# Optimization experiments

Hardware: AMD Instinct MI355X
Metric: run time of the kernel (lower is better)

Reference implementation:

```python
import jax, jax.numpy as jnp
import numpy as np

N = 50000      # nodes
E = 800000     # edges (avg degree 16)
IN = 128
H = 128
OUT = 1000
K = 10
EPS = 1e-5


def setup_inputs() -> dict:
    key = jax.random.key(0)
    ks = jax.random.split(key, 12)
    s = 0.05  # small init scale for weights
    return {
        "x": jax.random.normal(ks[0], (N, IN), jnp.float32),
        "edge_index": jax.random.randint(ks[1], (2, E), 0, N, dtype=jnp.int32),
        "W1": jax.random.normal(ks[2], (IN, H), jnp.float32) * s,
        "b1": jnp.zeros((H,), jnp.float32),
        "g1": jnp.ones((H,), jnp.float32),
        "be1": jnp.zeros((H,), jnp.float32),
        "W2": jax.random.normal(ks[3], (H, H), jnp.float32) * s,
        "b2": jnp.zeros((H,), jnp.float32),
        "g2": jnp.ones((H,), jnp.float32),
        "be2": jnp.zeros((H,), jnp.float32),
        "att": jax.random.uniform(ks[4], (K + 1,), jnp.float32),  # uniform_(0,1) init
        "W3": jax.random.normal(ks[5], (H, H // 2), jnp.float32) * s,
        "b3": jnp.zeros((H // 2,), jnp.float32),
        "g3": jnp.ones((H // 2,), jnp.float32),
        "be3": jnp.zeros((H // 2,), jnp.float32),
        "Wout": jax.random.normal(ks[6], (H // 2, OUT), jnp.float32) * s,
        "bout": jnp.zeros((OUT,), jnp.float32),
    }


def _bn(x, g, b):
    # training-mode BatchNorm1d: biased batch stats over the node dim
    m = jnp.mean(x, axis=0)
    v = jnp.var(x, axis=0)
    return g * (x - m) * jax.lax.rsqrt(v + EPS) + b


def reference(x, edge_index, W1, b1, g1, be1, W2, b2, g2, be2, att,
              W3, b3, g3, be3, Wout, bout):
    # input MLP with residual
    h = jax.nn.relu(_bn(x @ W1 + b1, g1, be1))
    identity = h
    h = jax.nn.relu(_bn(h @ W2 + b2, g2, be2)) + identity

    # DAGNN: K unnormalized scatter-add hops (APPNP.propagate with edge_weight=1),
    # then softmax(att)-weighted sum over hop representations. Accumulate the
    # weighted sum on the fly instead of materializing the [N, H, K+1] stack.
    src, dst = edge_index[0], edge_index[1]  # message flows src -> dst
    w = jax.nn.softmax(att)
    out = w[0] * h
    cur = h
    for i in range(K):
        cur = jax.ops.segment_sum(cur[src], dst, num_segments=N)
        out = out + w[i + 1] * cur

    # output MLP
    h3 = jax.nn.relu(_bn(out @ W3 + b3, g3, be3))
    return h3 @ Wout + bout
```

## Files before the change

### kernel.cpp

```cpp
#include <hip/hip_runtime.h>
#include <cstdint>
#include <cstddef>

#define N_NODES 50000
#define N_EDGES 800000
#define DIM_H   128
#define DIM_P   64
#define DIM_OUT 1000
#define OUT_PAD 1024
#define KHOPS   10
#define BN_EPS  1e-5f

static inline int ceil_div(int a, int b) { return (a + b - 1) / b; }

typedef short  bf16x8  __attribute__((ext_vector_type(8)));
typedef float  floatx4 __attribute__((ext_vector_type(4)));

__device__ __forceinline__ unsigned short f2bf_rne(float v) {
    unsigned int u = __float_as_uint(v);
    return (unsigned short)((u + 0x7fffu + ((u >> 16) & 1u)) >> 16);
}
__device__ __forceinline__ float bf2f(unsigned short u) {
    return __uint_as_float((unsigned int)u << 16);
}

__global__ void init_all(const float* __restrict__ att, float* __restrict__ w,
                         const float* __restrict__ Wout, unsigned short* __restrict__ WT,
                         double* __restrict__ st, int* __restrict__ deg) {
    const int gid = blockIdx.x * blockDim.x + threadIdx.x;
    const int stride = gridDim.x * blockDim.x;
    if (gid == 0) {
        float mx = att[0];
        for (int i = 1; i < KHOPS + 1; ++i) mx = fmaxf(mx, att[i]);
        float e[KHOPS + 1];
        float s = 0.f;
        for (int i = 0; i < KHOPS + 1; ++i) { e[i] = expf(att[i] - mx); s += e[i]; }
        for (int i = 0; i < KHOPS + 1; ++i) w[i] = e[i] / s;
    }
    for (int i = gid; i < 640; i += stride) st[i] = 0.0;
    for (int i = gid; i < N_NODES; i += stride) deg[i] = 0;
    for (int i = gid; i < OUT_PAD * DIM_P; i += stride) {
        int c = i >> 6, k = i & 63;
        WT[i] = (c < DIM_OUT) ? f2bf_rne(Wout[(size_t)k * DIM_OUT + c]) : (unsigned short)0;
    }
}

__global__ void count_deg(const int* __restrict__ dst, int* __restrict__ deg, int ne) {
    int i = blockIdx.x * blockDim.x + threadIdx.x;
    if (i < ne) atomicAdd(&deg[dst[i]], 1);
}

__global__ __launch_bounds__(1024) void scan_local(const int* __restrict__ deg,
                                                   int* __restrict__ row_ptr,
                                                   int* __restrict__ bsums, int n) {
    __shared__ int wsum[16];
    const int i = blockIdx.x * 1024 + threadIdx.x;
    const int lane = threadIdx.x & 63, w = threadIdx.x >> 6;
    int v = (i < n) ? deg[i] : 0;
    int s = v;
#pragma unroll
    for (int d = 1; d < 64; d <<= 1) {
        int t = __shfl_up(s, d, 64);
        if (lane >= d) s += t;
    }
    if (lane == 63) wsum[w] = s;
    __syncthreads();
    if (w == 0) {
        int x = (lane < 16) ? wsum[lane] : 0;
#pragma unroll
        for (int d = 1; d < 16; d <<= 1) {
            int t = __shfl_up(x, d, 64);
            if (lane >= d) x += t;
        }
        if (lane < 16) wsum[lane] = x;
    }
    __syncthreads();
    int incl = s + ((w > 0) ? wsum[w - 1] : 0);
    if (i < n) row_ptr[i + 1] = incl;
    if (threadIdx.x == 1023) bsums[blockIdx.x] = incl;
}

__global__ void scan_finish(int* __restrict__ row_ptr, int* __restrict__ deg,
                            const int* __restrict__ bsums, int n, int nb) {
    __shared__ int boff[64];
    if (threadIdx.x < 64) {
        int lane = threadIdx.x;
        int v = (lane < nb) ? bsums[lane] : 0;
        int s = v;
#pragma unroll
        for (int d = 1; d < 64; d <<= 1) {
            int t = __shfl_up(s, d, 64);
            if (lane >= d) s += t;
        }
        boff[lane] = s - v;
    }
    __syncthreads();
    int i = blockIdx.x * blockDim.x + threadIdx.x;
    if (i < n) {
        int incl = row_ptr[i + 1] + boff[i >> 10];
        row_ptr[i + 1] = incl;
        deg[i] = incl - deg[i];
    }
    if (i == 0) row_ptr[0] = 0;
}

__global__ void fill_csr(const int* __restrict__ src, const int* __restrict__ dst,
                         int* __restrict__ cursor, int* __restrict__ col, int ne) {
    int i = blockIdx.x * blockDim.x + threadIdx.x;
    if (i < ne) {
        int d = dst[i];
        int pos = atomicAdd(&cursor[d], 1);
        col[pos] = src[i];
    }
}

template<int KD, int CPB, bool OBF>
__global__ __launch_bounds__(256) void gemm_fused(
    const float* __restrict__ A,  const double* __restrict__ stA,
    const float* __restrict__ gA, const float* __restrict__ beA,
    const float* __restrict__ A2, const double* __restrict__ stA2,
    const float* __restrict__ gA2, const float* __restrict__ beA2,
    const float* __restrict__ W,
    float* __restrict__ C, int n, int M) {
    constexpr int CG  = CPB / 4;
    constexpr int RG  = 256 / CG;
    constexpr int RPT = 64 / RG;
    __shared__ float As[64][KD + 4];
    __shared__ float scA_l[2][KD];
    __shared__ float scA2_l[2][KD];

    const int tid  = threadIdx.x;
    const int cg   = tid % CG;
    const int rg   = tid / CG;
    const int row0 = blockIdx.x * 64;
    const int col0 = blockIdx.y * CPB + cg * 4;

    if (stA && tid < KD) {
        double m = stA[tid] / n;
        double v = stA[KD + tid] / n - m * m;
        float scale = gA[tid] * rsqrtf((float)v + BN_EPS);
        scA_l[0][tid] = scale;
        scA_l[1][tid] = beA[tid] - (float)m * scale;
    }
    if (A2 && tid < KD) {
        double m = stA2[tid] / n;
        double v = stA2[KD + tid] / n - m * m;
        float scale = gA2[tid] * rsqrtf((float)v + BN_EPS);
        scA2_l[0][tid] = scale;
        scA2_l[1][tid] = beA2[tid] - (float)m * scale;
    }
    if (stA || A2) __syncthreads();

    constexpr int VECS = 64 * KD / 4;
    for (int i = tid; i < VECS; i += 256) {
        int r  = i / (KD / 4);
        int k4 = (i % (KD / 4)) * 4;
        float4 v = make_float4(0.f, 0.f, 0.f, 0.f);
        int row = row0 + r;
        if (row < n) {
            v = *reinterpret_cast<const float4*>(A + (size_t)row * KD + k4);
            if (stA) {
                float4 sc = *reinterpret_cast<const float4*>(&scA_l[0][k4]);
                float4 sh = *reinterpret_cast<const float4*>(&scA_l[1][k4]);
                v.x = fmaxf(v.x * sc.x + sh.x, 0.f);
                v.y = fmaxf(v.y * sc.y + sh.y, 0.f);
                v.z = fmaxf(v.z * sc.z + sh.z, 0.f);
                v.w = fmaxf(v.w * sc.w + sh.w, 0.f);
            }
            if (A2) {
                float4 u  = *reinterpret_cast<const float4*>(A2 + (size_t)row * KD + k4);
                float4 sc = *reinterpret_cast<const float4*>(&scA2_l[0][k4]);
                float4 sh = *reinterpret_cast<const float4*>(&scA2_l[1][k4]);
                v.x += fmaxf(u.x * sc.x + sh.x, 0.f);
                v.y += fmaxf(u.y * sc.y + sh.y, 0.f);
                v.z += fmaxf(u.z * sc.z + sh.z, 0.f);
                v.w += fmaxf(u.w * sc.w + sh.w, 0.f);
            }
        }
        *reinterpret_cast<float4*>(&As[r][k4]) = v;
    }
    __syncthreads();

    if (col0 >= M) return;

    float acc[RPT][4];
#pragma unroll
    for (int r = 0; r < RPT; ++r)
#pragma unroll
        for (int c = 0; c < 4; ++c) acc[r][c] = 0.f;

    for (int k4 = 0; k4 < KD; k4 += 4) {
        float4 w0 = *reinterpret_cast<const float4*>(W + (size_t)(k4 + 0) * M + col0);
        float4 w1 = *reinterpret_cast<const float4*>(W + (size_t)(k4 + 1) * M + col0);
        float4 w2 = *reinterpret_cast<const float4*>(W + (size_t)(k4 + 2) * M + col0);
        float4 w3 = *reinterpret_cast<const float4*>(W + (size_t)(k4 + 3) * M + col0);
#pragma unroll
        for (int r = 0; r < RPT; ++r) {
            float4 a = *reinterpret_cast<const float4*>(&As[rg * RPT + r][k4]);
            acc[r][0] += a.x * w0.x + a.y * w1.x + a.z * w2.x + a.w * w3.x;
            acc[r][1] += a.x * w0.y + a.y * w1.y + a.z * w2.y + a.w * w3.y;
            acc[r][2] += a.x * w0.z + a.y * w1.z + a.z * w2.z + a.w * w3.z;
            acc[r][3] += a.x * w0.w + a.y * w1.w + a.z * w2.w + a.w * w3.w;
        }
    }

#pragma unroll
    for (int r = 0; r < RPT; ++r) {
        int row = row0 + rg * RPT + r;
        if (row < n) {
            float4 o = make_float4(acc[r][0], acc[r][1], acc[r][2], acc[r][3]);
            if (OBF) {
                unsigned short* cb = reinterpret_cast<unsigned short*>(C);
                ushort4 p;
                p.x = f2bf_rne(o.x); p.y = f2bf_rne(o.y);
                p.z = f2bf_rne(o.z); p.w = f2bf_rne(o.w);
                *reinterpret_cast<ushort4*>(cb + (size_t)row * M + col0) = p;
            } else {
                *reinterpret_cast<float4*>(C + (size_t)row * M + col0) = o;
            }
        }
    }
}

template<int M>
__global__ __launch_bounds__(256) void colstats(const float* __restrict__ Z,
                                                double* __restrict__ st, int n) {
    constexpr int RG = 256 / M;
    const int tid = threadIdx.x;
    const int c = tid % M, rg = tid / M;
    double s = 0.0, ss = 0.0;
    for (int row = blockIdx.x * RG + rg; row < n; row += gridDim.x * RG) {
        float v = Z[(size_t)row * M + c];
        s += v;
        ss += (double)v * (double)v;
    }
    __shared__ double sh[2][256];
    sh[0][tid] = s;
    sh[1][tid] = ss;
    __syncthreads();
    if (rg == 0) {
#pragma unroll
        for (int g = 1; g < RG; ++g) { s += sh[0][c + g * M]; ss += sh[1][c + g * M]; }
        atomicAdd(&st[c], s);
        atomicAdd(&st[M + c], ss);
    }
}

__global__ __launch_bounds__(256) void propagate(
    const unsigned short* __restrict__ cur, unsigned short* __restrict__ nxt,
    const int* __restrict__ row_ptr, const int* __restrict__ col, int n) {
    const int node = blockIdx.x * 4 + (threadIdx.x >> 6);
    const int lane = threadIdx.x & 63;
    const int g = lane >> 3;
    const int l = lane & 7;
    if (node >= n) return;
    const int beg = row_ptr[node], end = row_ptr[node + 1];
    float acc[8];
#pragma unroll
    for (int j = 0; j < 8; ++j) acc[j] = 0.f;

    int e = beg;
    for (; e + 16 <= end; e += 16) {
        int s0 = col[e + g];
        int s1 = col[e + g + 8];
        bf16x8 v0 = *reinterpret_cast<const bf16x8*>(cur + (size_t)s0 * DIM_P + l * 8);
        bf16x8 v1 = *reinterpret_cast<const bf16x8*>(cur + (size_t)s1 * DIM_P + l * 8);
#pragma unroll
        for (int j = 0; j < 8; ++j)
            acc[j] += bf2f((unsigned short)v0[j]) + bf2f((unsigned short)v1[j]);
    }
    if (e + 8 <= end) {
        int s = col[e + g];
        bf16x8 v = *reinterpret_cast<const bf16x8*>(cur + (size_t)s * DIM_P + l * 8);
#pragma unroll
        for (int j = 0; j < 8; ++j) acc[j] += bf2f((unsigned short)v[j]);
        e += 8;
    }
    if (e + g < end) {
        int s = col[e + g];
        bf16x8 v = *reinterpret_cast<const bf16x8*>(cur + (size_t)s * DIM_P + l * 8);
#pragma unroll
        for (int j = 0; j < 8; ++j) acc[j] += bf2f((unsigned short)v[j]);
    }

#pragma unroll
    for (int off = 8; off < 64; off <<= 1) {
#pragma unroll
        for (int j = 0; j < 8; ++j) acc[j] += __shfl_xor(acc[j], off, 64);
    }

    if (g == 0) {
        bf16x8 ov;
#pragma unroll
        for (int j = 0; j < 8; ++j) ov[j] = (short)f2bf_rne(acc[j]);
        *reinterpret_cast<bf16x8*>(nxt + (size_t)node * DIM_P + l * 8) = ov;
    }
}

__global__ __launch_bounds__(256) void wsum_stats(
    const unsigned short* __restrict__ hs, const float* __restrict__ wts,
    float* __restrict__ oa, double* __restrict__ st, int n) {
    const int tid = threadIdx.x;
    const int c = tid & 63, rg = tid >> 6;
    float w[KHOPS + 1];
#pragma unroll
    for (int i = 0; i < KHOPS + 1; ++i) w[i] = wts[i];
    const size_t stride = (size_t)n * DIM_P;
    double s = 0.0, ss = 0.0;
    for (int row = blockIdx.x * 4 + rg; row < n; row += gridDim.x * 4) {
        const size_t idx = (size_t)row * DIM_P + c;
        float val = 0.f;
#pragma unroll
        for (int i = 0; i < KHOPS + 1; ++i)
            val += w[i] * bf2f(hs[idx + (size_t)i * stride]);
        oa[idx] = val;
        s += val;
        ss += (double)val * (double)val;
    }
    __shared__ double sh[2][256];
    sh[0][tid] = s;
    sh[1][tid] = ss;
    __syncthreads();
    if (rg == 0) {
#pragma unroll
        for (int g2 = 1; g2 < 4; ++g2) { s += sh[0][c + g2 * 64]; ss += sh[1][c + g2 * 64]; }
        atomicAdd(&st[c], s);
        atomicAdd(&st[64 + c], ss);
    }
}

__global__ __launch_bounds__(256, 4) void out_gemm_mfma(
    const float* __restrict__ oa, const double* __restrict__ st3,
    const float* __restrict__ g3, const float* __restrict__ be3,
    const unsigned short* __restrict__ WT,
    const float* __restrict__ bout, float* __restrict__ out) {
    __shared__ float sc[DIM_P], sh[DIM_P];
    if (threadIdx.x < DIM_P) {
        int c = threadIdx.x;
        double m = st3[c] / N_NODES;
        double v = st3[DIM_P + c] / N_NODES - m * m;
        float scale = g3[c] * rsqrtf((float)v + BN_EPS);
        sc[c] = scale;
        sh[c] = be3[c] - (float)m * scale;
    }
    __syncthreads();

    const int wave = threadIdx.x >> 6;
    const int lane = threadIdx.x & 63;
    const int m    = lane & 15;
    const int quad = lane >> 4;
    const int kb   = quad * 8;
    const int c0   = blockIdx.y * 256 + wave * 64;

    bf16x8 afrag[4][2];
    float4 bias[4];
#pragma unroll
    for (int t = 0; t < 4; ++t) {
        const unsigned short* wrow = WT + (size_t)(c0 + t * 16 + m) * DIM_P;
        afrag[t][0] = *reinterpret_cast<const bf16x8*>(wrow + kb);
        afrag[t][1] = *reinterpret_cast<const bf16x8*>(wrow + 32 + kb);
        int cc = c0 + t * 16 + quad * 4;
        bias[t] = (cc < DIM_OUT) ? *reinterpret_cast<const float4*>(bout + cc)
                                 : make_float4(0.f, 0.f, 0.f, 0.f);
    }

    const int NT = N_NODES / 16;
    for (int rt = blockIdx.x; rt < NT; rt += gridDim.x) {
        const int row = rt * 16 + m;
        const float* arow = oa + (size_t)row * DIM_P;
        bf16x8 bfrag[2];
#pragma unroll
        for (int kh = 0; kh < 2; ++kh) {
            const int k0 = kh * 32 + kb;
            float4 a0 = *reinterpret_cast<const float4*>(arow + k0);
            float4 a1 = *reinterpret_cast<const float4*>(arow + k0 + 4);
            float4 s0 = *reinterpret_cast<const float4*>(&sc[k0]);
            float4 s1 = *reinterpret_cast<const float4*>(&sc[k0 + 4]);
            float4 h0 = *reinterpret_cast<const float4*>(&sh[k0]);
            float4 h1 = *reinterpret_cast<const float4*>(&sh[k0 + 4]);
            bfrag[kh][0] = (short)f2bf_rne(fmaxf(a0.x * s0.x + h0.x, 0.f));
            bfrag[kh][1] = (short)f2bf_rne(fmaxf(a0.y * s0.y + h0.y, 0.f));
            bfrag[kh][2] = (short)f2bf_rne(fmaxf(a0.z * s0.z + h0.z, 0.f));
            bfrag[kh][3] = (short)f2bf_rne(fmaxf(a0.w * s0.w + h0.w, 0.f));
            bfrag[kh][4] = (short)f2bf_rne(fmaxf(a1.x * s1.x + h1.x, 0.f));
            bfrag[kh][5] = (short)f2bf_rne(fmaxf(a1.y * s1.y + h1.y, 0.f));
            bfrag[kh][6] = (short)f2bf_rne(fmaxf(a1.z * s1.z + h1.z, 0.f));
            bfrag[kh][7] = (short)f2bf_rne(fmaxf(a1.w * s1.w + h1.w, 0.f));
        }
        float* orow = out + (size_t)row * DIM_OUT;
#pragma unroll
        for (int t = 0; t < 4; ++t) {
            floatx4 acc = {0.f, 0.f, 0.f, 0.f};
            acc = __builtin_amdgcn_mfma_f32_16x16x32_bf16(afrag[t][0], bfrag[0], acc, 0, 0, 0);
            acc = __builtin_amdgcn_mfma_f32_16x16x32_bf16(afrag[t][1], bfrag[1], acc, 0, 0, 0);
            int cc = c0 + t * 16 + quad * 4;
            if (cc < DIM_OUT) {
                float4 o = make_float4(acc[0] + bias[t].x, acc[1] + bias[t].y,
                                       acc[2] + bias[t].z, acc[3] + bias[t].w);
                *reinterpret_cast<float4*>(orow + cc) = o;
            }
        }
    }
}

extern "C" void kernel_launch(void* const* d_in, const int* in_sizes, int n_in,
                              void* d_out, int out_size, void* d_ws, size_t ws_size,
                              hipStream_t stream) {
    const float* x    = (const float*)d_in[0];
    const int*   ei   = (const int*)  d_in[1];
    const float* W1   = (const float*)d_in[2];
    const float* g1   = (const float*)d_in[4];
    const float* be1  = (const float*)d_in[5];
    const float* W2   = (const float*)d_in[6];
    const float* g2   = (const float*)d_in[8];
    const float* be2  = (const float*)d_in[9];
    const float* att  = (const float*)d_in[10];
    const float* W3   = (const float*)d_in[11];
    const float* g3   = (const float*)d_in[13];
    const float* be3  = (const float*)d_in[14];
    const float* Wout = (const float*)d_in[15];
    const float* bout = (const float*)d_in[16];
    float* out = (float*)d_out;

    char* base = (char*)d_ws;
    size_t off = 0;
    auto alloc = [&](size_t bytes) -> void* {
        void* r = base + off;
        off += (bytes + 255) & ~(size_t)255;
        return r;
    };
    const size_t SSTRIDE = (size_t)N_NODES * DIM_P;
    float*  f0      = (float*) alloc((size_t)N_NODES * DIM_H * 4);
    float*  f1      = (float*) alloc((size_t)N_NODES * DIM_H * 4);
    unsigned short* hs = (unsigned short*)alloc((size_t)(KHOPS + 1) * SSTRIDE * 2);
    float*  oa      = (float*) alloc(SSTRIDE * 4);
    double* st      = (double*)alloc(640 * 8);
    float*  wts     = (float*) alloc(16 * 4);
    int*    row_ptr = (int*)   alloc((size_t)(N_NODES + 1) * 4);
    int*    deg     = (int*)   alloc((size_t)N_NODES * 4);
    int*    col     = (int*)   alloc((size_t)N_EDGES * 4);
    int*    bsums   = (int*)   alloc(64 * 4);
    unsigned short* WT = (unsigned short*)alloc((size_t)OUT_PAD * DIM_P * 2);

    const int* src = ei;
    const int* dst = ei + N_EDGES;
    double* st1 = st;   double* st2 = st + 256; double* st3 = st + 512;

    init_all<<<256, 256, 0, stream>>>(att, wts, Wout, WT, st, deg);

    count_deg<<<ceil_div(N_EDGES, 256), 256, 0, stream>>>(dst, deg, N_EDGES);
    const int NB = ceil_div(N_NODES, 1024);
    scan_local<<<NB, 1024, 0, stream>>>(deg, row_ptr, bsums, N_NODES);
    scan_finish<<<ceil_div(N_NODES, 256), 256, 0, stream>>>(row_ptr, deg, bsums,
                                                            N_NODES, NB);
    fill_csr<<<ceil_div(N_EDGES, 256), 256, 0, stream>>>(src, dst, deg, col, N_EDGES);

    const int RB = ceil_div(N_NODES, 64);

    gemm_fused<128, 128, false><<<dim3(RB, 1), 256, 0, stream>>>(
        x, nullptr, nullptr, nullptr,
        nullptr, nullptr, nullptr, nullptr,
        W1, f0, N_NODES, DIM_H);
    colstats<128><<<256, 256, 0, stream>>>(f0, st1, N_NODES);

    gemm_fused<128, 128, false><<<dim3(RB, 1), 256, 0, stream>>>(
        f0, st1, g1, be1,
        nullptr, nullptr, nullptr, nullptr,
        W2, f1, N_NODES, DIM_H);
    colstats<128><<<256, 256, 0, stream>>>(f1, st2, N_NODES);

    gemm_fused<128, 64, true><<<dim3(RB, 1), 256, 0, stream>>>(
        f1, st2, g2, be2,
        f0, st1, g1, be1,
        W3, (float*)hs, N_NODES, DIM_P);

    for (int hop = 1; hop <= KHOPS; ++hop) {
        propagate<<<ceil_div(N_NODES, 4), 256, 0, stream>>>(
            hs + (size_t)(hop - 1) * SSTRIDE, hs + (size_t)hop * SSTRIDE,
            row_ptr, col, N_NODES);
    }

    wsum_stats<<<256, 256, 0, stream>>>(hs, wts, oa, st3, N_NODES);

    out_gemm_mfma<<<dim3(512, 4), 256, 0, stream>>>(oa, st3, g3, be3, WT, bout, out);
}
```

Baseline: 759.6 us.

## Replace FP32 FMA GEMMs with split-bf16 MFMA GEMMs for input MLP layers

```diff
diff --git a/kernel.cpp b/kernel.cpp
--- a/kernel.cpp
+++ b/kernel.cpp
@@ -26,6 +26,12 @@
 
 __global__ void init_all(const float* __restrict__ att, float* __restrict__ w,
                          const float* __restrict__ Wout, unsigned short* __restrict__ WT,
+                         const float* __restrict__ W1, unsigned short* __restrict__ WT1h,
+                         unsigned short* __restrict__ WT1l,
+                         const float* __restrict__ W2, unsigned short* __restrict__ WT2h,
+                         unsigned short* __restrict__ WT2l,
+                         const float* __restrict__ W3, unsigned short* __restrict__ WT3h,
+                         unsigned short* __restrict__ WT3l,
                          double* __restrict__ st, int* __restrict__ deg) {
     const int gid = blockIdx.x * blockDim.x + threadIdx.x;
     const int stride = gridDim.x * blockDim.x;
@@ -43,6 +49,24 @@
         int c = i >> 6, k = i & 63;
         WT[i] = (c < DIM_OUT) ? f2bf_rne(Wout[(size_t)k * DIM_OUT + c]) : (unsigned short)0;
     }
+    for (int i = gid; i < DIM_H * DIM_H; i += stride) {
+        int m = i >> 7, k = i & 127;
+        float w1v = W1[(size_t)k * DIM_H + m];
+        unsigned short h1 = f2bf_rne(w1v);
+        WT1h[i] = h1;
+        WT1l[i] = f2bf_rne(w1v - bf2f(h1));
+        float w2v = W2[(size_t)k * DIM_H + m];
+        unsigned short h2 = f2bf_rne(w2v);
+        WT2h[i] = h2;
+        WT2l[i] = f2bf_rne(w2v - bf2f(h2));
+    }
+    for (int i = gid; i < DIM_P * DIM_H; i += stride) {
+        int m = i >> 7, k = i & 127;
+        float w3v = W3[(size_t)k * DIM_P + m];
+        unsigned short h3 = f2bf_rne(w3v);
+        WT3h[i] = h3;
+        WT3l[i] = f2bf_rne(w3v - bf2f(h3));
+    }
 }
 
 __global__ void count_deg(const int* __restrict__ dst, int* __restrict__ deg, int ne) {
@@ -114,109 +138,137 @@
     }
 }
 
-template<int KD, int CPB, bool OBF>
-__global__ __launch_bounds__(256) void gemm_fused(
+template<int M, bool DUAL, bool OBF>
+__global__ __launch_bounds__(256) void gemm_mfma_split(
     const float* __restrict__ A,  const double* __restrict__ stA,
     const float* __restrict__ gA, const float* __restrict__ beA,
     const float* __restrict__ A2, const double* __restrict__ stA2,
     const float* __restrict__ gA2, const float* __restrict__ beA2,
-    const float* __restrict__ W,
-    float* __restrict__ C, int n, int M) {
-    constexpr int CG  = CPB / 4;
-    constexpr int RG  = 256 / CG;
-    constexpr int RPT = 64 / RG;
-    __shared__ float As[64][KD + 4];
-    __shared__ float scA_l[2][KD];
-    __shared__ float scA2_l[2][KD];
+    const unsigned short* __restrict__ WTh, const unsigned short* __restrict__ WTl,
+    float* __restrict__ C, int n) {
+    constexpr int K  = 128;
+    constexpr int CT = M / 64;
+    __shared__ __align__(16) unsigned short Ah[64][K + 8];
+    __shared__ __align__(16) unsigned short Al[64][K + 8];
+    __shared__ __align__(16) float scl[2][K];
+    __shared__ __align__(16) float scl2[2][K];
 
     const int tid  = threadIdx.x;
-    const int cg   = tid % CG;
-    const int rg   = tid / CG;
+    const int wave = tid >> 6;
+    const int lane = tid & 63;
+    const int m15  = lane & 15;
+    const int quad = lane >> 4;
     const int row0 = blockIdx.x * 64;
-    const int col0 = blockIdx.y * CPB + cg * 4;
-
-    if (stA && tid < KD) {
-        double m = stA[tid] / n;
-        double v = stA[KD + tid] / n - m * m;
-        float scale = gA[tid] * rsqrtf((float)v + BN_EPS);
-        scA_l[0][tid] = scale;
-        scA_l[1][tid] = beA[tid] - (float)m * scale;
-    }
-    if (A2 && tid < KD) {
-        double m = stA2[tid] / n;
-        double v = stA2[KD + tid] / n - m * m;
-        float scale = gA2[tid] * rsqrtf((float)v + BN_EPS);
-        scA2_l[0][tid] = scale;
-        scA2_l[1][tid] = beA2[tid] - (float)m * scale;
-    }
-    if (stA || A2) __syncthreads();
-
-    constexpr int VECS = 64 * KD / 4;
-    for (int i = tid; i < VECS; i += 256) {
-        int r  = i / (KD / 4);
-        int k4 = (i % (KD / 4)) * 4;
+
+    if (stA && tid < K) {
+        double mm = stA[tid] / n;
+        double vv = stA[K + tid] / n - mm * mm;
+        float scale = gA[tid] * rsqrtf((float)vv + BN_EPS);
+        scl[0][tid] = scale;
+        scl[1][tid] = beA[tid] - (float)mm * scale;
+    }
+    if (DUAL && tid < K) {
+        double mm = stA2[tid] / n;
+        double vv = stA2[K + tid] / n - mm * mm;
+        float scale = gA2[tid] * rsqrtf((float)vv + BN_EPS);
+        scl2[0][tid] = scale;
+        scl2[1][tid] = beA2[tid] - (float)mm * scale;
+    }
+    __syncthreads();
+
+    for (int i = tid; i < 64 * 32; i += 256) {
+        int r  = i >> 5;
+        int k4 = (i & 31) * 4;
         float4 v = make_float4(0.f, 0.f, 0.f, 0.f);
         int row = row0 + r;
         if (row < n) {
-            v = *reinterpret_cast<const float4*>(A + (size_t)row * KD + k4);
+            v = *reinterpret_cast<const float4*>(A + (size_t)row * K + k4);
             if (stA) {
-                float4 sc = *reinterpret_cast<const float4*>(&scA_l[0][k4]);
-                float4 sh = *reinterpret_cast<const float4*>(&scA_l[1][k4]);
+                float4 sc = *reinterpret_cast<const float4*>(&scl[0][k4]);
+                float4 sh = *reinterpret_cast<const float4*>(&scl[1][k4]);
                 v.x = fmaxf(v.x * sc.x + sh.x, 0.f);
                 v.y = fmaxf(v.y * sc.y + sh.y, 0.f);
                 v.z = fmaxf(v.z * sc.z + sh.z, 0.f);
                 v.w = fmaxf(v.w * sc.w + sh.w, 0.f);
             }
-            if (A2) {
-                float4 u  = *reinterpret_cast<const float4*>(A2 + (size_t)row * KD + k4);
-                float4 sc = *reinterpret_cast<const float4*>(&scA2_l[0][k4]);
-                float4 sh = *reinterpret_cast<const float4*>(&scA2_l[1][k4]);
+            if (DUAL) {
+                float4 u  = *reinterpret_cast<const float4*>(A2 + (size_t)row * K + k4);
+                float4 sc = *reinterpret_cast<const float4*>(&scl2[0][k4]);
+                float4 sh = *reinterpret_cast<const float4*>(&scl2[1][k4]);
                 v.x += fmaxf(u.x * sc.x + sh.x, 0.f);
                 v.y += fmaxf(u.y * sc.y + sh.y, 0.f);
                 v.z += fmaxf(u.z * sc.z + sh.z, 0.f);
                 v.w += fmaxf(u.w * sc.w + sh.w, 0.f);
             }
         }
-        *reinterpret_cast<float4*>(&As[r][k4]) = v;
-    }
-    __syncthreads();
-
-    if (col0 >= M) return;
-
-    float acc[RPT][4];
-#pragma unroll
-    for (int r = 0; r < RPT; ++r)
-#pragma unroll
-        for (int c = 0; c < 4; ++c) acc[r][c] = 0.f;
-
-    for (int k4 = 0; k4 < KD; k4 += 4) {
-        float4 w0 = *reinterpret_cast<const float4*>(W + (size_t)(k4 + 0) * M + col0);
-        float4 w1 = *reinterpret_cast<const float4*>(W + (size_t)(k4 + 1) * M + col0);
-        float4 w2 = *reinterpret_cast<const float4*>(W + (size_t)(k4 + 2) * M + col0);
-        float4 w3 = *reinterpret_cast<const float4*>(W + (size_t)(k4 + 3) * M + col0);
-#pragma unroll
-        for (int r = 0; r < RPT; ++r) {
-            float4 a = *reinterpret_cast<const float4*>(&As[rg * RPT + r][k4]);
-            acc[r][0] += a.x * w0.x + a.y * w1.x + a.z * w2.x + a.w * w3.x;
-            acc[r][1] += a.x * w0.y + a.y * w1.y + a.z * w2.y + a.w * w3.y;
-            acc[r][2] += a.x * w0.z + a.y * w1.z + a.z * w2.z + a.w * w3.z;
-            acc[r][3] += a.x * w0.w + a.y * w1.w + a.z * w2.w + a.w * w3.w;
-        }
-    }
-
-#pragma unroll
-    for (int r = 0; r < RPT; ++r) {
-        int row = row0 + rg * RPT + r;
-        if (row < n) {
-            float4 o = make_float4(acc[r][0], acc[r][1], acc[r][2], acc[r][3]);
-            if (OBF) {
-                unsigned short* cb = reinterpret_cast<unsigned short*>(C);
-                ushort4 p;
-                p.x = f2bf_rne(o.x); p.y = f2bf_rne(o.y);
-                p.z = f2bf_rne(o.z); p.w = f2bf_rne(o.w);
-                *reinterpret_cast<ushort4*>(cb + (size_t)row * M + col0) = p;
-            } else {
-                *reinterpret_cast<float4*>(C + (size_t)row * M + col0) = o;
+        ushort4 ph, pl;
+        ph.x = f2bf_rne(v.x); pl.x = f2bf_rne(v.x - bf2f(ph.x));
+        ph.y = f2bf_rne(v.y); pl.y = f2bf_rne(v.y - bf2f(ph.y));
+        ph.z = f2bf_rne(v.z); pl.z = f2bf_rne(v.z - bf2f(ph.z));
+        ph.w = f2bf_rne(v.w); pl.w = f2bf_rne(v.w - bf2f(ph.w));
+        *reinterpret_cast<ushort4*>(&Ah[r][k4]) = ph;
+        *reinterpret_cast<ushort4*>(&Al[r][k4]) = pl;
+    }
+    __syncthreads();
+
+    bf16x8 afh[CT][4], afl[CT][4];
+#pragma unroll
+    for (int t = 0; t < CT; ++t) {
+        const size_t wroff = (size_t)(wave * CT * 16 + t * 16 + m15) * K + quad * 8;
+#pragma unroll
+        for (int ch = 0; ch < 4; ++ch) {
+            afh[t][ch] = *reinterpret_cast<const bf16x8*>(WTh + wroff + ch * 32);
+            afl[t][ch] = *reinterpret_cast<const bf16x8*>(WTl + wroff + ch * 32);
+        }
+    }
+
+    floatx4 acc[CT][4];
+#pragma unroll
+    for (int t = 0; t < CT; ++t)
+#pragma unroll
+        for (int rt = 0; rt < 4; ++rt) acc[t][rt] = (floatx4){0.f, 0.f, 0.f, 0.f};
+
+#pragma unroll
+    for (int rt = 0; rt < 4; ++rt) {
+        bf16x8 bfh[4], bfl[4];
+#pragma unroll
+        for (int ch = 0; ch < 4; ++ch) {
+            bfh[ch] = *reinterpret_cast<const bf16x8*>(&Ah[rt * 16 + m15][ch * 32 + quad * 8]);
+            bfl[ch] = *reinterpret_cast<const bf16x8*>(&Al[rt * 16 + m15][ch * 32 + quad * 8]);
+        }
+#pragma unroll
+        for (int t = 0; t < CT; ++t)
+#pragma unroll
+            for (int ch = 0; ch < 4; ++ch) {
+                acc[t][rt] = __builtin_amdgcn_mfma_f32_16x16x32_bf16(
+                    afh[t][ch], bfh[ch], acc[t][rt], 0, 0, 0);
+                acc[t][rt] = __builtin_amdgcn_mfma_f32_16x16x32_bf16(
+                    afl[t][ch], bfh[ch], acc[t][rt], 0, 0, 0);
+                acc[t][rt] = __builtin_amdgcn_mfma_f32_16x16x32_bf16(
+                    afh[t][ch], bfl[ch], acc[t][rt], 0, 0, 0);
+            }
+    }
+
+#pragma unroll
+    for (int t = 0; t < CT; ++t) {
+        const int c = wave * CT * 16 + t * 16 + quad * 4;
+#pragma unroll
+        for (int rt = 0; rt < 4; ++rt) {
+            int row = row0 + rt * 16 + m15;
+            if (row < n) {
+                if (OBF) {
+                    unsigned short* cb = reinterpret_cast<unsigned short*>(C);
+                    ushort4 p;
+                    p.x = f2bf_rne(acc[t][rt][0]);
+                    p.y = f2bf_rne(acc[t][rt][1]);
+                    p.z = f2bf_rne(acc[t][rt][2]);
+                    p.w = f2bf_rne(acc[t][rt][3]);
+                    *reinterpret_cast<ushort4*>(cb + (size_t)row * M + c) = p;
+                } else {
+                    float4 o = make_float4(acc[t][rt][0], acc[t][rt][1],
+                                           acc[t][rt][2], acc[t][rt][3]);
+                    *reinterpret_cast<float4*>(C + (size_t)row * M + c) = o;
+                }
             }
         }
     }
@@ -440,13 +492,21 @@
     int*    deg     = (int*)   alloc((size_t)N_NODES * 4);
     int*    col     = (int*)   alloc((size_t)N_EDGES * 4);
     int*    bsums   = (int*)   alloc(64 * 4);
-    unsigned short* WT = (unsigned short*)alloc((size_t)OUT_PAD * DIM_P * 2);
+    unsigned short* WT   = (unsigned short*)alloc((size_t)OUT_PAD * DIM_P * 2);
+    unsigned short* WT1h = (unsigned short*)alloc((size_t)DIM_H * DIM_H * 2);
+    unsigned short* WT1l = (unsigned short*)alloc((size_t)DIM_H * DIM_H * 2);
+    unsigned short* WT2h = (unsigned short*)alloc((size_t)DIM_H * DIM_H * 2);
+    unsigned short* WT2l = (unsigned short*)alloc((size_t)DIM_H * DIM_H * 2);
+    unsigned short* WT3h = (unsigned short*)alloc((size_t)DIM_P * DIM_H * 2);
+    unsigned short* WT3l = (unsigned short*)alloc((size_t)DIM_P * DIM_H * 2);
 
     const int* src = ei;
     const int* dst = ei + N_EDGES;
     double* st1 = st;   double* st2 = st + 256; double* st3 = st + 512;
 
-    init_all<<<256, 256, 0, stream>>>(att, wts, Wout, WT, st, deg);
+    init_all<<<256, 256, 0, stream>>>(att, wts, Wout, WT,
+                                      W1, WT1h, WT1l, W2, WT2h, WT2l,
+                                      W3, WT3h, WT3l, st, deg);
 
     count_deg<<<ceil_div(N_EDGES, 256), 256, 0, stream>>>(dst, deg, N_EDGES);
     const int NB = ceil_div(N_NODES, 1024);
@@ -457,22 +517,22 @@
 
     const int RB = ceil_div(N_NODES, 64);
 
-    gemm_fused<128, 128, false><<<dim3(RB, 1), 256, 0, stream>>>(
+    gemm_mfma_split<128, false, false><<<dim3(RB), 256, 0, stream>>>(
         x, nullptr, nullptr, nullptr,
         nullptr, nullptr, nullptr, nullptr,
-        W1, f0, N_NODES, DIM_H);
+        WT1h, WT1l, f0, N_NODES);
     colstats<128><<<256, 256, 0, stream>>>(f0, st1, N_NODES);
 
-    gemm_fused<128, 128, false><<<dim3(RB, 1), 256, 0, stream>>>(
+    gemm_mfma_split<128, false, false><<<dim3(RB), 256, 0, stream>>>(
         f0, st1, g1, be1,
         nullptr, nullptr, nullptr, nullptr,
-        W2, f1, N_NODES, DIM_H);
+        WT2h, WT2l, f1, N_NODES);
     colstats<128><<<256, 256, 0, stream>>>(f1, st2, N_NODES);
 
-    gemm_fused<128, 64, true><<<dim3(RB, 1), 256, 0, stream>>>(
+    gemm_mfma_split<64, true, true><<<dim3(RB), 256, 0, stream>>>(
         f1, st2, g2, be2,
         f0, st1, g1, be1,
-        W3, (float*)hs, N_NODES, DIM_P);
+        WT3h, WT3l, (float*)hs, N_NODES);
 
     for (int hop = 1; hop <= KHOPS; ++hop) {
         propagate<<<ceil_div(N_NODES, 4), 256, 0, stream>>>(
```

Result: faster. 724.6 us (-4.6%).
